# Optimization experiments

Hardware: AMD Instinct MI355X
Metric: run time of the kernel (lower is better)

## Reference

```python
import jax, jax.numpy as jnp
import numpy as np

N_HEAD = 12

def setup_inputs() -> dict:
    key = jax.random.key(0)
    k1, k2, k3 = jax.random.split(key, 3)
    nx = 768
    B, S = 2, 2048
    return {
        "hidden_states": jax.random.normal(k1, (B, S, nx), dtype=jnp.float32),
        "w_attn": jax.random.normal(k2, (nx, 3 * nx), dtype=jnp.float32) * 0.02,
        "b_attn": jnp.zeros((3 * nx,), dtype=jnp.float32),
        "w_proj": jax.random.normal(k3, (nx, nx), dtype=jnp.float32) * 0.02,
        "b_proj": jnp.zeros((nx,), dtype=jnp.float32),
    }

def reference(hidden_states, w_attn, b_attn, w_proj, b_proj):
    B, S, nx = hidden_states.shape
    d_head = nx // N_HEAD
    qkv = hidden_states @ w_attn + b_attn  # [B,S,3nx]
    q, k, v = jnp.split(qkv, 3, axis=-1)
    # split heads -> [B,H,S,d]
    def split(x):
        return x.reshape(B, S, N_HEAD, d_head).transpose(0, 2, 1, 3)
    q, k, v = split(q), split(k), split(v)
    # scale=True: divide by sqrt(d_head) (v.size(-1))
    w = jnp.einsum("bhsd,bhtd->bhst", q, k) / jnp.sqrt(jnp.float32(d_head))
    w = jax.nn.softmax(w, axis=-1)
    a = jnp.einsum("bhst,bhtd->bhsd", w, v)  # [B,H,S,d]
    a = a.transpose(0, 2, 1, 3).reshape(B, S, nx)  # merge heads
    return a @ w_proj + b_proj
```

## Files before the change

kernel.cpp:

```cpp
#include <hip/hip_runtime.h>

#define NHEAD 12
#define DHEAD 64
#define SEQ   2048
#define NB    2
#define NX    768
#define MTOK  (NB * SEQ)

typedef __attribute__((ext_vector_type(8))) short short8;
typedef __attribute__((ext_vector_type(4))) short short4v;
typedef __attribute__((ext_vector_type(4))) float f32x4;

__device__ __forceinline__ unsigned short f2bf(float x) {
    union { float f; unsigned u; } v; v.f = x;
    unsigned r = v.u + 0x7fffu + ((v.u >> 16) & 1u);
    return (unsigned short)(r >> 16);
}

#define MFMA32(a, b, c) __builtin_amdgcn_mfma_f32_16x16x32_bf16(a, b, c, 0, 0, 0)
#define MFMA16(a, b, c) __builtin_amdgcn_mfma_f32_16x16x16bf16_1k(a, b, c, 0, 0, 0)

__global__ __launch_bounds__(256)
void cvt_k(const float* __restrict__ X, unsigned short* __restrict__ Y, int n4)
{
    int i = blockIdx.x * 256 + threadIdx.x;
    if (i >= n4) return;
    float4 v = ((const float4*)X)[i];
    ushort4 o;
    o.x = f2bf(v.x); o.y = f2bf(v.y); o.z = f2bf(v.z); o.w = f2bf(v.w);
    ((ushort4*)Y)[i] = o;
}

__global__ __launch_bounds__(256)
void cvtT_k(const float* __restrict__ W, unsigned short* __restrict__ T, int K, int N)
{
    __shared__ float tile[32][33];
    const int t = threadIdx.x;
    const int r = t >> 5, c = t & 31;
    const int k0 = blockIdx.y * 32, n0 = blockIdx.x * 32;
#pragma unroll
    for (int i = 0; i < 4; i++)
        tile[r + i * 8][c] = W[(size_t)(k0 + r + i * 8) * N + n0 + c];
    __syncthreads();
#pragma unroll
    for (int i = 0; i < 4; i++) {
        int n = r + i * 8;
        T[(size_t)(n0 + n) * K + k0 + c] = f2bf(tile[c][n]);
    }
}

template<int MODE>
__global__ __launch_bounds__(256, 3)
void gemm_bf(const unsigned short* __restrict__ A,
             const unsigned short* __restrict__ Bt,
             const float* __restrict__ bias,
             float* __restrict__ fo,
             unsigned short* __restrict__ qb, unsigned short* __restrict__ kb2,
             unsigned short* __restrict__ vtb,
             int M, int N, int K)
{
    __shared__ __align__(16) unsigned char sm[2][16384];
    const int t = threadIdx.x;
    const int w = t >> 6, lane = t & 63;
    const int lo16 = lane & 15, quad = lane >> 4;
    const int ib = blockIdx.y * 128, jb = blockIdx.x * 128;

    f32x4 acc[4][4];
#pragma unroll
    for (int mt = 0; mt < 4; mt++)
#pragma unroll
        for (int nt = 0; nt < 4; nt++) acc[mt][nt] = (f32x4){0.f, 0.f, 0.f, 0.f};

    const int srow = lane >> 2;
    const int sj   = lane & 3;

    auto stage = [&](int buf, int k0) {
#pragma unroll
        for (int i = 0; i < 4; i++) {
            const int u   = i * 4 + w;
            const int p   = u >> 3;
            const int row = (u & 7) * 16 + srow;
            const int sc  = sj ^ (row & 3);
            const unsigned short* g = (p == 0)
                ? (A  + (size_t)(ib + row) * K + k0 + sc * 8)
                : (Bt + (size_t)(jb + row) * K + k0 + sc * 8);
            void* lp = &sm[buf][p * 8192 + (u & 7) * 1024];
            __builtin_amdgcn_global_load_lds(
                (const __attribute__((address_space(1))) unsigned int*)g,
                (__attribute__((address_space(3))) unsigned int*)lp, 16, 0, 0);
        }
    };

    const int mrow = (w >> 1) * 64;
    const int nrow = (w & 1) * 64;

    stage(0, 0);
    const int NIT = K / 32;
    for (int kt = 0; kt < NIT; kt++) {
        const int buf = kt & 1;
        __syncthreads();
        if (kt + 1 < NIT) stage(buf ^ 1, (kt + 1) * 32);

        short8 af[4], bf[4];
#pragma unroll
        for (int mt = 0; mt < 4; mt++) {
            const int row = mrow + mt * 16 + lo16;
            af[mt] = *(const short8*)&sm[buf][row * 64 + ((quad ^ (row & 3)) * 16)];
        }
#pragma unroll
        for (int nt = 0; nt < 4; nt++) {
            const int row = nrow + nt * 16 + lo16;
            bf[nt] = *(const short8*)&sm[buf][8192 + row * 64 + ((quad ^ (row & 3)) * 16)];
        }
#pragma unroll
        for (int mt = 0; mt < 4; mt++)
#pragma unroll
            for (int nt = 0; nt < 4; nt++)
                acc[mt][nt] = MFMA32(af[mt], bf[nt], acc[mt][nt]);
    }

    if constexpr (MODE == 0) {
        const int which = jb / NX;
#pragma unroll
        for (int nt = 0; nt < 4; nt++) {
            const int j  = jb + nrow + nt * 16 + lo16;
            const int cc = j - which * NX;
            const int hh = cc >> 6, dd = cc & 63;
            const float bj = bias[j];
#pragma unroll
            for (int mt = 0; mt < 4; mt++) {
                const int m0 = ib + mrow + mt * 16 + quad * 4;
                const int bb = m0 >> 11;
                const int s0 = m0 & 2047;
                const size_t hb = (size_t)(bb * NHEAD + hh);
                if (which == 2) {
                    ushort4 pv;
                    pv.x = f2bf(acc[mt][nt][0] + bj);
                    pv.y = f2bf(acc[mt][nt][1] + bj);
                    pv.z = f2bf(acc[mt][nt][2] + bj);
                    pv.w = f2bf(acc[mt][nt][3] + bj);
                    *(ushort4*)(vtb + (hb * DHEAD + dd) * SEQ + s0) = pv;
                } else {
                    unsigned short* dst = (which == 0) ? qb : kb2;
                    const float sc = (which == 0) ? 0.125f : 1.0f;
#pragma unroll
                    for (int r = 0; r < 4; r++)
                        dst[(hb * SEQ + s0 + r) * DHEAD + dd] =
                            f2bf((acc[mt][nt][r] + bj) * sc);
                }
            }
        }
    } else {
#pragma unroll
        for (int nt = 0; nt < 4; nt++) {
            const int j  = jb + nrow + nt * 16 + lo16;
            const float bj = bias[j];
#pragma unroll
            for (int mt = 0; mt < 4; mt++) {
                const int m0 = ib + mrow + mt * 16 + quad * 4;
#pragma unroll
                for (int r = 0; r < 4; r++)
                    fo[(size_t)(m0 + r) * N + j] = acc[mt][nt][r] + bj;
            }
        }
    }
}

__global__ __launch_bounds__(256, 3)
void attn_bf(const unsigned short* __restrict__ qb, const unsigned short* __restrict__ kb,
             const unsigned short* __restrict__ vtb, unsigned short* __restrict__ ab)
{
    __shared__ __align__(16) unsigned char sm[2][16384];
    const int t = threadIdx.x;
    const int w = t >> 6, lane = t & 63;
    const int lo16 = lane & 15, quad = lane >> 4;

    const int id = blockIdx.x;
    const int xcd = id & 7, slot = id >> 3;
    const int bh = xcd * 3 + slot % 3;
    const int q0 = (slot / 3) * 64;
    const int b = bh / NHEAD, h = bh % NHEAD;

    const unsigned short* Qb = qb  + (size_t)bh * SEQ * DHEAD;
    const unsigned short* Kb = kb  + (size_t)bh * SEQ * DHEAD;
    const unsigned short* Vb = vtb + (size_t)bh * DHEAD * SEQ;

    short8 qf[2];
    {
        const size_t qo = (size_t)(q0 + w * 16 + lo16) * DHEAD + quad * 8;
        qf[0] = *(const short8*)(Qb + qo);
        qf[1] = *(const short8*)(Qb + qo + 32);
    }

    const int srow = lane >> 3;
    const int sj   = lane & 7;
    auto stage = [&](int buf, int k0) {
#pragma unroll
        for (int i = 0; i < 4; i++) {
            const int u   = i * 4 + w;
            const int p   = u >> 3;
            const int row = (u & 7) * 8 + srow;
            const int sc  = sj ^ (row & 7);
            const unsigned short* g = (p == 0)
                ? (Kb + (size_t)(k0 + row) * DHEAD + sc * 8)
                : (Vb + (size_t)row * SEQ + k0 + sc * 8);
            void* lp = &sm[buf][p * 8192 + (u & 7) * 1024];
            __builtin_amdgcn_global_load_lds(
                (const __attribute__((address_space(1))) unsigned int*)g,
                (__attribute__((address_space(3))) unsigned int*)lp, 16, 0, 0);
        }
    };

    f32x4 oacc[4];
#pragma unroll
    for (int dt = 0; dt < 4; dt++) oacc[dt] = (f32x4){0.f, 0.f, 0.f, 0.f};
    float lsum = 0.f;

    stage(0, 0);
    for (int kt = 0; kt < SEQ / 64; kt++) {
        const int buf = kt & 1;
        __syncthreads();
        if (kt + 1 < SEQ / 64) stage(buf ^ 1, (kt + 1) * 64);

        f32x4 s[4];
#pragma unroll
        for (int rt = 0; rt < 4; rt++) {
            const int row = rt * 16 + lo16;
            const int rs = row & 7;
            short8 kf0 = *(const short8*)&sm[buf][row * 128 + ((quad ^ rs) * 16)];
            short8 kf1 = *(const short8*)&sm[buf][row * 128 + (((4 + quad) ^ rs) * 16)];
            f32x4 a = (f32x4){0.f, 0.f, 0.f, 0.f};
            a = MFMA32(kf0, qf[0], a);
            a = MFMA32(kf1, qf[1], a);
            s[rt] = a;
        }

        short4v pf[4];
#pragma unroll
        for (int rt = 0; rt < 4; rt++) {
            float p0 = __expf(s[rt][0]), p1 = __expf(s[rt][1]);
            float p2 = __expf(s[rt][2]), p3 = __expf(s[rt][3]);
            lsum += (p0 + p1) + (p2 + p3);
            short4v pv;
            pv[0] = (short)f2bf(p0); pv[1] = (short)f2bf(p1);
            pv[2] = (short)f2bf(p2); pv[3] = (short)f2bf(p3);
            pf[rt] = pv;
        }

#pragma unroll
        for (int dt = 0; dt < 4; dt++) {
            const int row = dt * 16 + lo16;
            const int rs = row & 7;
            f32x4 a = oacc[dt];
#pragma unroll
            for (int rt = 0; rt < 4; rt++) {
                const int ch = (2 * rt + (quad >> 1)) ^ rs;
                short4v vf = *(const short4v*)&sm[buf][8192 + row * 128 + ch * 16 + (quad & 1) * 8];
                a = MFMA16(vf, pf[rt], a);
            }
            oacc[dt] = a;
        }
    }

    lsum += __shfl_xor(lsum, 16);
    lsum += __shfl_xor(lsum, 32);
    const float inv = 1.0f / lsum;

    unsigned short* dst = ab + (size_t)(b * SEQ + q0 + w * 16 + lo16) * NX + h * DHEAD;
#pragma unroll
    for (int dt = 0; dt < 4; dt++) {
        ushort4 pv;
        pv.x = f2bf(oacc[dt][0] * inv);
        pv.y = f2bf(oacc[dt][1] * inv);
        pv.z = f2bf(oacc[dt][2] * inv);
        pv.w = f2bf(oacc[dt][3] * inv);
        *(ushort4*)(dst + dt * 16 + quad * 4) = pv;
    }
}

extern "C" void kernel_launch(void* const* d_in, const int* in_sizes, int n_in,
                              void* d_out, int out_size, void* d_ws, size_t ws_size,
                              hipStream_t stream)
{
    const float* hs     = (const float*)d_in[0];
    const float* w_attn = (const float*)d_in[1];
    const float* b_attn = (const float*)d_in[2];
    const float* w_proj = (const float*)d_in[3];
    const float* b_proj = (const float*)d_in[4];
    float* out = (float*)d_out;

    unsigned short* wsu = (unsigned short*)d_ws;
    unsigned short* Abf  = wsu;
    unsigned short* WtA  = Abf  + 3145728;
    unsigned short* WtP  = WtA  + 1769472;
    unsigned short* qbuf = WtP  + 589824;
    unsigned short* kbuf = qbuf + 3145728;
    unsigned short* vtbf = kbuf + 3145728;
    unsigned short* abf  = vtbf + 3145728;

    cvt_k<<<3072, 256, 0, stream>>>(hs, Abf, 786432);
    cvtT_k<<<dim3(72, 24), 256, 0, stream>>>(w_attn, WtA, NX, 3 * NX);
    cvtT_k<<<dim3(24, 24), 256, 0, stream>>>(w_proj, WtP, NX, NX);

    gemm_bf<0><<<dim3(18, 32), 256, 0, stream>>>(
        Abf, WtA, b_attn, nullptr, qbuf, kbuf, vtbf, MTOK, 3 * NX, NX);

    attn_bf<<<768, 256, 0, stream>>>(qbuf, kbuf, vtbf, abf);

    gemm_bf<1><<<dim3(6, 32), 256, 0, stream>>>(
        abf, WtP, b_proj, out, nullptr, nullptr, nullptr, MTOK, NX, NX);
}
```

Baseline: 163.5 us.

## Split attention keys across waves with register-direct loads and LDS reduction

The attention kernel no longer stages K/V tiles through double-buffered LDS. Each wave now handles all 64 queries of the block against its own 16-key slice of every 64-key tile, loading K and V straight from global memory into registers with one-tile prefetch. Partial outputs and row sums are combined across waves through shared memory at the end. Softmax uses exp2 with log2e folded into the Q scale, and bf16 packing uses byte-permute truncation instead of round-to-nearest. This removes the per-tile barriers and LDS traffic, but it adds more uncoalesced global loads, more accumulator registers, and a final cross-wave reduction, and truncation slightly changes numerics.

```diff
diff --git a/kernel.cpp b/kernel.cpp
--- a/kernel.cpp
+++ b/kernel.cpp
@@ -142,7 +142,7 @@
                     *(ushort4*)(vtb + (hb * DHEAD + dd) * SEQ + s0) = pv;
                 } else {
                     unsigned short* dst = (which == 0) ? qb : kb2;
-                    const float sc = (which == 0) ? 0.125f : 1.0f;
+                    const float sc = (which == 0) ? 0.1803368801f : 1.0f;
 #pragma unroll
                     for (int r = 0; r < 4; r++)
                         dst[(hb * SEQ + s0 + r) * DHEAD + dd] =
@@ -170,7 +170,8 @@
 void attn_bf(const unsigned short* __restrict__ qb, const unsigned short* __restrict__ kb,
              const unsigned short* __restrict__ vtb, unsigned short* __restrict__ ab)
 {
-    __shared__ __align__(16) unsigned char sm[2][16384];
+    __shared__ float red[12544];
+
     const int t = threadIdx.x;
     const int w = t >> 6, lane = t & 63;
     const int lo16 = lane & 15, quad = lane >> 4;
@@ -185,96 +186,120 @@
     const unsigned short* Kb = kb  + (size_t)bh * SEQ * DHEAD;
     const unsigned short* Vb = vtb + (size_t)bh * DHEAD * SEQ;
 
-    short8 qf[2];
-    {
-        const size_t qo = (size_t)(q0 + w * 16 + lo16) * DHEAD + quad * 8;
-        qf[0] = *(const short8*)(Qb + qo);
-        qf[1] = *(const short8*)(Qb + qo + 32);
-    }
-
-    const int srow = lane >> 3;
-    const int sj   = lane & 7;
-    auto stage = [&](int buf, int k0) {
-#pragma unroll
-        for (int i = 0; i < 4; i++) {
-            const int u   = i * 4 + w;
-            const int p   = u >> 3;
-            const int row = (u & 7) * 8 + srow;
-            const int sc  = sj ^ (row & 7);
-            const unsigned short* g = (p == 0)
-                ? (Kb + (size_t)(k0 + row) * DHEAD + sc * 8)
-                : (Vb + (size_t)row * SEQ + k0 + sc * 8);
-            void* lp = &sm[buf][p * 8192 + (u & 7) * 1024];
-            __builtin_amdgcn_global_load_lds(
-                (const __attribute__((address_space(1))) unsigned int*)g,
-                (__attribute__((address_space(3))) unsigned int*)lp, 16, 0, 0);
-        }
-    };
-
-    f32x4 oacc[4];
-#pragma unroll
-    for (int dt = 0; dt < 4; dt++) oacc[dt] = (f32x4){0.f, 0.f, 0.f, 0.f};
-    float lsum = 0.f;
-
-    stage(0, 0);
+    short8 qf[4][2];
+#pragma unroll
+    for (int qt = 0; qt < 4; qt++) {
+        const unsigned short* qp = Qb + (size_t)(q0 + qt * 16 + lo16) * DHEAD + quad * 8;
+        qf[qt][0] = *(const short8*)qp;
+        qf[qt][1] = *(const short8*)(qp + 32);
+    }
+
+    f32x4 oacc[4][4];
+#pragma unroll
+    for (int dt = 0; dt < 4; dt++)
+#pragma unroll
+        for (int qt = 0; qt < 4; qt++) oacc[dt][qt] = (f32x4){0.f, 0.f, 0.f, 0.f};
+    float lsum[4] = {0.f, 0.f, 0.f, 0.f};
+
+    const unsigned short* kp = Kb + (size_t)(w * 16 + lo16) * DHEAD + quad * 8;
+    const unsigned short* vp = Vb + (size_t)lo16 * SEQ + w * 16 + quad * 4;
+
+    short8 kc0 = *(const short8*)kp;
+    short8 kc1 = *(const short8*)(kp + 32);
+    short4v vc[4];
+#pragma unroll
+    for (int dt = 0; dt < 4; dt++) vc[dt] = *(const short4v*)(vp + (size_t)dt * 16 * SEQ);
+
+    const unsigned sel = 0x07060302u;
+
     for (int kt = 0; kt < SEQ / 64; kt++) {
-        const int buf = kt & 1;
-        __syncthreads();
-        if (kt + 1 < SEQ / 64) stage(buf ^ 1, (kt + 1) * 64);
+        const int ktn = (kt < SEQ / 64 - 1) ? kt + 1 : kt;
+        const unsigned short* kpn = kp + (size_t)ktn * 64 * DHEAD;
+        const unsigned short* vpn = vp + (size_t)ktn * 64;
+        short8 kn0 = *(const short8*)kpn;
+        short8 kn1 = *(const short8*)(kpn + 32);
+        short4v vn[4];
+#pragma unroll
+        for (int dt = 0; dt < 4; dt++) vn[dt] = *(const short4v*)(vpn + (size_t)dt * 16 * SEQ);
 
         f32x4 s[4];
 #pragma unroll
-        for (int rt = 0; rt < 4; rt++) {
-            const int row = rt * 16 + lo16;
-            const int rs = row & 7;
-            short8 kf0 = *(const short8*)&sm[buf][row * 128 + ((quad ^ rs) * 16)];
-            short8 kf1 = *(const short8*)&sm[buf][row * 128 + (((4 + quad) ^ rs) * 16)];
+        for (int qt = 0; qt < 4; qt++) {
             f32x4 a = (f32x4){0.f, 0.f, 0.f, 0.f};
-            a = MFMA32(kf0, qf[0], a);
-            a = MFMA32(kf1, qf[1], a);
-            s[rt] = a;
+            a = MFMA32(kc0, qf[qt][0], a);
+            a = MFMA32(kc1, qf[qt][1], a);
+            s[qt] = a;
         }
 
         short4v pf[4];
 #pragma unroll
-        for (int rt = 0; rt < 4; rt++) {
-            float p0 = __expf(s[rt][0]), p1 = __expf(s[rt][1]);
-            float p2 = __expf(s[rt][2]), p3 = __expf(s[rt][3]);
-            lsum += (p0 + p1) + (p2 + p3);
-            short4v pv;
-            pv[0] = (short)f2bf(p0); pv[1] = (short)f2bf(p1);
-            pv[2] = (short)f2bf(p2); pv[3] = (short)f2bf(p3);
-            pf[rt] = pv;
-        }
-
-#pragma unroll
-        for (int dt = 0; dt < 4; dt++) {
-            const int row = dt * 16 + lo16;
-            const int rs = row & 7;
-            f32x4 a = oacc[dt];
-#pragma unroll
-            for (int rt = 0; rt < 4; rt++) {
-                const int ch = (2 * rt + (quad >> 1)) ^ rs;
-                short4v vf = *(const short4v*)&sm[buf][8192 + row * 128 + ch * 16 + (quad & 1) * 8];
-                a = MFMA16(vf, pf[rt], a);
-            }
-            oacc[dt] = a;
-        }
-    }
-
-    lsum += __shfl_xor(lsum, 16);
-    lsum += __shfl_xor(lsum, 32);
-    const float inv = 1.0f / lsum;
-
-    unsigned short* dst = ab + (size_t)(b * SEQ + q0 + w * 16 + lo16) * NX + h * DHEAD;
+        for (int qt = 0; qt < 4; qt++) {
+            union { float f; unsigned u; } p0, p1, p2, p3;
+            p0.f = __builtin_amdgcn_exp2f(s[qt][0]);
+            p1.f = __builtin_amdgcn_exp2f(s[qt][1]);
+            p2.f = __builtin_amdgcn_exp2f(s[qt][2]);
+            p3.f = __builtin_amdgcn_exp2f(s[qt][3]);
+            lsum[qt] += (p0.f + p1.f) + (p2.f + p3.f);
+            union { unsigned u[2]; short4v v; } pk;
+            pk.u[0] = __builtin_amdgcn_perm(p1.u, p0.u, sel);
+            pk.u[1] = __builtin_amdgcn_perm(p3.u, p2.u, sel);
+            pf[qt] = pk.v;
+        }
+
+#pragma unroll
+        for (int dt = 0; dt < 4; dt++)
+#pragma unroll
+            for (int qt = 0; qt < 4; qt++)
+                oacc[dt][qt] = MFMA16(vc[dt], pf[qt], oacc[dt][qt]);
+
+        kc0 = kn0; kc1 = kn1;
+#pragma unroll
+        for (int dt = 0; dt < 4; dt++) vc[dt] = vn[dt];
+    }
+
+#pragma unroll
+    for (int qt = 0; qt < 4; qt++) {
+        lsum[qt] += __shfl_xor(lsum[qt], 16);
+        lsum[qt] += __shfl_xor(lsum[qt], 32);
+    }
+    if (quad == 0) {
+#pragma unroll
+        for (int qt = 0; qt < 4; qt++)
+            red[12288 + w * 64 + qt * 16 + lo16] = lsum[qt];
+    }
+
 #pragma unroll
     for (int dt = 0; dt < 4; dt++) {
-        ushort4 pv;
-        pv.x = f2bf(oacc[dt][0] * inv);
-        pv.y = f2bf(oacc[dt][1] * inv);
-        pv.z = f2bf(oacc[dt][2] * inv);
-        pv.w = f2bf(oacc[dt][3] * inv);
-        *(ushort4*)(dst + dt * 16 + quad * 4) = pv;
+        if (dt == w) continue;
+        const int sl = dt - (dt > w ? 1 : 0);
+#pragma unroll
+        for (int qt = 0; qt < 4; qt++)
+            *(f32x4*)&red[((w * 3 + sl) * 64 + qt * 16 + lo16) * 16 + quad * 4] = oacc[dt][qt];
+    }
+    __syncthreads();
+
+#pragma unroll
+    for (int ow = 0; ow < 4; ow++) {
+        if (ow == w) continue;
+        const int sl = w - (w > ow ? 1 : 0);
+#pragma unroll
+        for (int qt = 0; qt < 4; qt++)
+            oacc[w][qt] += *(const f32x4*)&red[((ow * 3 + sl) * 64 + qt * 16 + lo16) * 16 + quad * 4];
+    }
+
+#pragma unroll
+    for (int qt = 0; qt < 4; qt++) {
+        const int q = qt * 16 + lo16;
+        const float lt = red[12288 + q] + red[12288 + 64 + q]
+                       + red[12288 + 128 + q] + red[12288 + 192 + q];
+        const float inv = 1.0f / lt;
+        f32x4 o = oacc[w][qt] * inv;
+        union { float f; unsigned u; } a0, a1, a2, a3;
+        a0.f = o[0]; a1.f = o[1]; a2.f = o[2]; a3.f = o[3];
+        uint2 pk;
+        pk.x = __builtin_amdgcn_perm(a1.u, a0.u, sel);
+        pk.y = __builtin_amdgcn_perm(a3.u, a2.u, sel);
+        *(uint2*)(ab + (size_t)(b * SEQ + q0 + q) * NX + h * DHEAD + w * 16 + quad * 4) = pk;
     }
 }
 
```

New measurement: 207.1 us. 26.7% more time.
